# Kernel tuning notes

Measured on AMD Instinct MI355X. Metric: run time of the kernel, lower is better.

Reference implementation:

```python
import jax, jax.numpy as jnp
import numpy as np

LRELU_GAIN = 2.0 ** 0.5  # util.lrelu_gain (assumed sqrt(2))
EPS = 1e-8


def upsample2_bilinear_ac(x):
    # F.upsample_bilinear == bilinear with align_corners=True, scale 2
    B, C, H, W = x.shape
    def lerp_axis(t, n, axis):
        c = jnp.arange(2 * n, dtype=jnp.float32) * (n - 1) / (2 * n - 1)
        i0 = jnp.floor(c).astype(jnp.int32)
        i1 = jnp.minimum(i0 + 1, n - 1)
        f = c - i0.astype(jnp.float32)
        a = jnp.take(t, i0, axis=axis)
        b = jnp.take(t, i1, axis=axis)
        shape = [1] * t.ndim
        shape[axis] = 2 * n
        f = f.reshape(shape)
        return a * (1.0 - f) + b * f
    x = lerp_axis(x, H, 2)
    x = lerp_axis(x, W, 3)
    return x


def conv1x1(x, weight, bias, gain):
    # Conv2dNormalizedLR with kernel_size=1: he = gain/sqrt(in)
    cin = weight.shape[1]
    he = gain / float(cin) ** 0.5
    y = jnp.einsum('bihw,oi->bohw', x, weight[:, :, 0, 0] * he)
    return y + bias[None, :, None, None]


def mod_conv3x3(x, weight, style, gain):
    # weight: [Cin, Cout, 3, 3]; style: [B, Cin]
    cin, cout, k, _ = weight.shape
    he = gain / float(cin * k * k) ** 0.5
    wmod = style[:, :, None, None, None] * (weight * he)[None]  # [B,Cin,Cout,k,k]
    # demodulation: normalize over (in, kh, kw) per out channel
    d = jax.lax.rsqrt(jnp.sum(wmod * wmod, axis=(1, 3, 4), keepdims=True) + EPS)
    wmod = wmod * d
    # conv_transpose2d(stride=1, pad=1, k=3) == conv2d with transposed+flipped kernel, pad=1
    kern = jnp.flip(jnp.transpose(wmod, (0, 2, 1, 3, 4)), axis=(3, 4))  # [B,Cout,Cin,k,k]
    def one(xb, kb):
        return jax.lax.conv_general_dilated(
            xb[None], kb, (1, 1), ((1, 1), (1, 1)),
            dimension_numbers=('NCHW', 'OIHW', 'NCHW'))[0]
    y = jax.vmap(one)(x, kern)
    return y * gain


def noise_affine(noise, w_s, b_s, w_b, b_b):
    # Baff*: 1x1 conv from 1 channel, gain=1 -> he=1
    ys = noise * w_s[None, :, 0, None, 0, None][:, :, :, 0] if False else noise * w_s[:, 0, 0, 0][None, :, None, None] + b_s[None, :, None, None]
    yb = noise * w_b[:, 0, 0, 0][None, :, None, None] + b_b[None, :, None, None]
    return ys, yb


def block_forward(x, w, noise1, noise2, conv1_w, bias1, conv2_w, bias2,
                  Aaff1_w, Aaff1_b, Aaff2_w, Aaff2_b,
                  Baff1s_w, Baff1s_b, Baff1b_w, Baff1b_b,
                  Baff2s_w, Baff2s_b, Baff2b_w, Baff2b_b,
                  rgb_w, rgb_b):
    x = upsample2_bilinear_ac(x)
    style1 = conv1x1(w, Aaff1_w, Aaff1_b, 1.0)[:, :, 0, 0]  # [B, Cin]
    x = mod_conv3x3(x, conv1_w, style1, LRELU_GAIN)
    ys, yb = noise_affine(noise1, Baff1s_w, Baff1s_b, Baff1b_w, Baff1b_b)
    x = x * ys + yb + bias1
    x = jax.nn.leaky_relu(x, 0.2)
    style2 = conv1x1(w, Aaff2_w, Aaff2_b, 1.0)[:, :, 0, 0]
    x = mod_conv3x3(x, conv2_w, style2, LRELU_GAIN)
    ys, yb = noise_affine(noise2, Baff2s_w, Baff2s_b, Baff2b_w, Baff2b_b)
    x = x * ys + yb + bias2
    x = jax.nn.leaky_relu(x, 0.2)
    rgb = conv1x1(x, rgb_w, rgb_b, 0.03)
    return x, rgb


def setup_inputs() -> dict:
    key = jax.random.key(0)
    ks = jax.random.split(key, 20)
    B, Cin, Cout, Wd, H, W = 8, 512, 512, 512, 32, 32
    inp = {
        'x': jax.random.normal(ks[0], (B, Cin, H, W), jnp.float32),
        'w': jax.random.normal(ks[1], (B, Wd, 1, 1), jnp.float32),
        'noise1': jax.random.normal(ks[2], (B, 1, 2 * H, 2 * W), jnp.float32),
        'noise2': jax.random.normal(ks[3], (B, 1, 2 * H, 2 * W), jnp.float32),
        'conv1_w': jax.random.normal(ks[4], (Cin, Cout, 3, 3), jnp.float32),
        'bias1': jnp.zeros((1, Cout, 1, 1), jnp.float32),
        'conv2_w': jax.random.normal(ks[5], (Cout, Cout, 3, 3), jnp.float32),
        'bias2': jnp.zeros((1, Cout, 1, 1), jnp.float32),
        'Aaff1_w': jax.random.normal(ks[6], (Cin, Wd, 1, 1), jnp.float32),
        'Aaff1_b': jnp.zeros((Cin,), jnp.float32),
        'Aaff2_w': jax.random.normal(ks[7], (Cout, Wd, 1, 1), jnp.float32),
        'Aaff2_b': jnp.zeros((Cout,), jnp.float32),
        'Baff1s_w': jax.random.normal(ks[8], (Cout, 1, 1, 1), jnp.float32) * 0.1,
        'Baff1s_b': jnp.ones((Cout,), jnp.float32),
        'Baff1b_w': jax.random.normal(ks[9], (Cout, 1, 1, 1), jnp.float32) * 0.1,
        'Baff1b_b': jnp.zeros((Cout,), jnp.float32),
        'Baff2s_w': jax.random.normal(ks[10], (Cout, 1, 1, 1), jnp.float32) * 0.1,
        'Baff2s_b': jnp.ones((Cout,), jnp.float32),
        'Baff2b_w': jax.random.normal(ks[11], (Cout, 1, 1, 1), jnp.float32) * 0.1,
        'Baff2b_b': jnp.zeros((Cout,), jnp.float32),
        'rgb_w': jax.random.normal(ks[12], (3, Cout, 1, 1), jnp.float32),
        'rgb_b': jnp.zeros((3,), jnp.float32),
    }
    return inp


def reference(x, w, noise1, noise2, conv1_w, bias1, conv2_w, bias2,
              Aaff1_w, Aaff1_b, Aaff2_w, Aaff2_b,
              Baff1s_w, Baff1s_b, Baff1b_w, Baff1b_b,
              Baff2s_w, Baff2s_b, Baff2b_w, Baff2b_b,
              rgb_w, rgb_b):
    return block_forward(x, w, noise1, noise2, conv1_w, bias1, conv2_w, bias2,
                         Aaff1_w, Aaff1_b, Aaff2_w, Aaff2_b,
                         Baff1s_w, Baff1s_b, Baff1b_w, Baff1b_b,
                         Baff2s_w, Baff2s_b, Baff2b_w, Baff2b_b,
                         rgb_w, rgb_b)
```

## Files before the change

kernel.cpp:

```cpp
#include <hip/hip_runtime.h>
#include <hip/hip_bf16.h>

#define BB 8
#define CC 512
#define HO 64
#define HP 66
#define NPIX (BB*HO*HO)

typedef float f32x4 __attribute__((ext_vector_type(4)));
typedef __bf16 bf16x8 __attribute__((ext_vector_type(8)));
using bf16 = __hip_bfloat16;

__device__ __forceinline__ void gload16(const void* g, void* l) {
    __builtin_amdgcn_global_load_lds((const __attribute__((address_space(1))) void*)g,
                                     (__attribute__((address_space(3))) void*)l, 16, 0, 0);
}

__device__ __forceinline__ float waveRedSum(float v) {
    #pragma unroll
    for (int off = 32; off; off >>= 1) v += __shfl_down(v, off);
    return v;
}

__global__ void init_all(const float* __restrict__ W1, const float* __restrict__ W2,
                         float* __restrict__ S21, float* __restrict__ S22,
                         bf16* __restrict__ kT1, bf16* __restrict__ kT2, float he,
                         bf16* __restrict__ xs1, bf16* __restrict__ xs2,
                         const float* __restrict__ rgbb, float* __restrict__ outrgb) {
    int blk = blockIdx.x, tid = threadIdx.x;
    if (blk < 2048) {
        int which = blk >> 10;
        const float* Wsrc = which ? W2 : W1;
        float* S2ho = which ? S22 : S21;
        bf16* keffT = which ? kT2 : kT1;
        int t = ((blk & 1023) << 8) + tid;
        int i = t & (CC-1), o = t >> 9;
        const float* wp = Wsrc + (i*CC + o)*9;
        float v[9]; float s2 = 0.f;
        #pragma unroll
        for (int k = 0; k < 9; ++k) { v[k] = wp[k] * he; s2 += v[k]*v[k]; }
        S2ho[o*CC + i] = s2;
        #pragma unroll
        for (int tp = 0; tp < 9; ++tp) keffT[(tp*CC + o)*CC + i] = (bf16)v[8 - tp];
    } else if (blk < 3088) {
        int sub = ((blk - 2048) << 2) + (tid >> 6);
        int ln = tid & 63;
        bf16* dst = (sub & 1) ? xs2 : xs1;
        int idx = sub >> 1;
        int b = idx / 260, rm = idx - b*260;
        int p, q;
        if (rm < 66)       { p = 0;        q = rm; }
        else if (rm < 132) { p = 65;       q = rm - 66; }
        else if (rm < 196) { p = rm - 131; q = 0; }
        else               { p = rm - 195; q = 65; }
        f32x4* d4 = (f32x4*)(dst + ((size_t)((b*HP + p)*HP + q)) * CC);
        d4[ln] = f32x4{0.f, 0.f, 0.f, 0.f};
    } else {
        int t2 = ((blk - 3088) << 2) + (tid >> 6);
        int plane = t2 >> 4;
        int c = plane - (plane/3)*3;
        float v = rgbb[c];
        *(f32x4*)(outrgb + (plane << 12) + ((t2 & 15) << 8) + ((tid & 63) << 2)) =
            f32x4{v, v, v, v};
    }
}

__global__ void style_kernel(const float* __restrict__ w,
                             const float* __restrict__ A1, const float* __restrict__ A1b,
                             const float* __restrict__ A2, const float* __restrict__ A2b,
                             float* __restrict__ s1, float* __restrict__ s2) {
    int wid = (blockIdx.x * blockDim.x + threadIdx.x) >> 6;
    int lane = threadIdx.x & 63;
    int set = wid >= BB*CC; int rem = set ? wid - BB*CC : wid;
    int b = rem >> 9, i = rem & (CC-1);
    const float* A = set ? A2 : A1;
    const float* wb = w + b*CC;
    float sum = 0.f;
    for (int d = lane; d < CC; d += 64) sum += wb[d] * A[i*CC + d];
    sum = waveRedSum(sum);
    if (lane == 0) {
        float r = sum * 0.04419417382415922f + (set ? A2b : A1b)[i];
        (set ? s2 : s1)[b*CC + i] = r;
    }
}

__global__ void demod_kernel(const float* __restrict__ s1, const float* __restrict__ S21,
                             const float* __restrict__ s2, const float* __restrict__ S22,
                             float* __restrict__ dg1, float* __restrict__ dg2, float gain) {
    int wid = (blockIdx.x * blockDim.x + threadIdx.x) >> 6;
    int lane = threadIdx.x & 63;
    int set = wid >= BB*CC; int rem = set ? wid - BB*CC : wid;
    int b = rem >> 9, o = rem & (CC-1);
    const float* st = (set ? s2 : s1) + b*CC;
    const float* S2 = (set ? S22 : S21) + o*CC;
    float sum = 0.f;
    for (int i = lane; i < CC; i += 64) { float sv = st[i]; sum += sv*sv*S2[i]; }
    sum = waveRedSum(sum);
    if (lane == 0) (set ? dg2 : dg1)[b*CC + o] = gain * rsqrtf(sum + 1e-8f);
}

__global__ void upsample_mod(const float* __restrict__ x, const float* __restrict__ s1,
                             bf16* __restrict__ xs1) {
    __shared__ float usl[32][CC];
    int blk = blockIdx.x;
    int i = threadIdx.x;
    int b = blk >> 6, p = blk & 63;
    const float scale = 31.0f / 63.0f;
    float chf = p * scale; int h0 = (int)chf; float fh = chf - h0; int h1 = min(h0 + 1, 31);
    const float* xb = x + ((size_t)(b*CC + i) << 10);
    #pragma unroll
    for (int k = 0; k < 8; ++k) {
        f32x4 r0 = *(const f32x4*)(xb + (h0 << 5) + (k << 2));
        f32x4 r1 = *(const f32x4*)(xb + (h1 << 5) + (k << 2));
        #pragma unroll
        for (int e = 0; e < 4; ++e)
            usl[(k << 2) + e][i] = r0[e]*(1.f - fh) + r1[e]*fh;
    }
    float sv = s1[b*CC + i];
    bf16* op = xs1 + ((size_t)((b*HP + p + 1)*HP + 1))*CC + i;
    #pragma unroll
    for (int q = 0; q < 64; ++q) {
        float cwf = q * scale; int w0 = (int)cwf; float fw = cwf - w0;
        int w1 = min(w0 + 1, 31);
        float v = (usl[w0][i]*(1.f - fw) + usl[w1][i]*fw) * sv;
        op[q*CC] = (bf16)v;
    }
}

#define SB  __builtin_amdgcn_sched_barrier(0)
#define BAR __builtin_amdgcn_s_barrier()
#define VMC(n)  asm volatile("s_waitcnt vmcnt(" #n ")" ::: "memory")
#define LGKM(n) asm volatile("s_waitcnt lgkmcnt(" #n ")" ::: "memory")

#define STAGE_A(d, h, U) do { \
    gload16((U) + aThr + (h)*(HP*1024),                 ldsA + (d)*32768 + (h)*16384); \
    gload16((U) + aThr + (h)*(HP*1024) + 2*(HP*1024),   ldsA + (d)*32768 + (h)*16384 + 8192); \
} while (0)

#define STAGE_B(d, h, U) do { \
    gload16((U) + bThr + (h)*32768,                     ldsB + (d)*32768 + (h)*16384); \
    gload16((U) + bThr + (h)*32768 + 131072,            ldsB + (d)*32768 + (h)*16384 + 8192); \
} while (0)

#define LOAD_A(d, fh) do { \
    _Pragma("unroll") \
    for (int fmq = 0; fmq < 4; ++fmq) { \
        afr[fmq][0] = *(const bf16x8*)(aRd + (d)*32768 + (fh)*16384 + fmq*2048 + swz0); \
        afr[fmq][1] = *(const bf16x8*)(aRd + (d)*32768 + (fh)*16384 + fmq*2048 + swz1); \
    } } while (0)

#define LOAD_B(d, nh) do { \
    _Pragma("unroll") \
    for (int fnq = 0; fnq < 2; ++fnq) { \
        bfr[nh][fnq][0] = *(const bf16x8*)(bRd + (d)*32768 + (nh)*16384 + fnq*2048 + swz0); \
        bfr[nh][fnq][1] = *(const bf16x8*)(bRd + (d)*32768 + (nh)*16384 + fnq*2048 + swz1); \
    } } while (0)

#define QUAD(fh, nh) do { \
    __builtin_amdgcn_s_setprio(1); \
    _Pragma("unroll") \
    for (int kc = 0; kc < 2; ++kc) \
    { _Pragma("unroll") \
      for (int fmq = 0; fmq < 4; ++fmq) \
      { _Pragma("unroll") \
        for (int fnq = 0; fnq < 2; ++fnq) \
            acc[(fh)*4+fmq][(nh)*2+fnq] = __builtin_amdgcn_mfma_f32_16x16x32_bf16( \
                afr[fmq][kc], bfr[nh][fnq][kc], acc[(fh)*4+fmq][(nh)*2+fnq], 0, 0, 0); } } \
    __builtin_amdgcn_s_setprio(0); } while (0)

#define PHSTEP(cur, nxt, aN1, bN1, aN2, g1, g3) do { \
     \
    LOAD_A(cur, 0); \
    LOAD_B(cur, 0); \
    if (g1) STAGE_B(nxt, 0, bN1); \
    LGKM(8); SB; BAR; LGKM(0); SB; \
    QUAD(0, 0); \
    VMC(4); SB; BAR; SB; \
     \
    LOAD_B(cur, 1); \
    if (g1) STAGE_B(nxt, 1, bN1); \
    SB; BAR; LGKM(0); SB; \
    QUAD(0, 1); \
    SB; BAR; SB; \
     \
    LOAD_A(cur, 1); \
    if (g1) STAGE_A(nxt, 1, aN1); \
    SB; BAR; LGKM(0); SB; \
    QUAD(1, 1); \
    SB; BAR; SB; \
     \
    if (g3) STAGE_A(cur, 0, aN2); \
    SB; BAR; SB; \
    QUAD(1, 0); \
    if (g3) { VMC(6); } else { VMC(0); } \
    SB; BAR; SB; \
} while (0)

#define CONV_COMMON \
    __shared__ __attribute__((aligned(16))) bf16 As[32768]; \
    __shared__ __attribute__((aligned(16))) bf16 Bs[32768]; \
    const int tid = threadIdx.x; \
    const int wave = tid >> 6, lane = tid & 63; \
    const int tileId = ((blockIdx.x & 7) << 5) + (blockIdx.x >> 3); \
    const int mtile = tileId >> 1, ntile = tileId & 1; \
    const int m0 = mtile << 8, n0 = ntile << 8; \
    const int b  = m0 >> 12; \
    const int p0 = (m0 & 4095) >> 6; \
    const int wm = wave >> 2, wn = wave & 3; \
    const int l15 = lane & 15; \
    const int srcSwz = (((tid & 7) ^ ((tid >> 3) & 7)) << 4); \
    const int aThr = ((tid >> 3) << 10) + srcSwz; \
    const int bThr = (((tid >> 8) & 1) << 16) + (((tid >> 3) & 31) << 10) + srcSwz; \
    char* const ldsA = (char*)As + tid*16; \
    char* const ldsB = (char*)Bs + tid*16; \
    const char* const aRd = (const char*)As + (((wm << 6) + l15) << 7); \
    const char* const bRd = (const char*)Bs + (((wn << 5) + l15) << 7); \
    const int swz0 = (((lane >> 4)    ) ^ (lane & 7)) << 4; \
    const int swz1 = (((lane >> 4) | 4) ^ (lane & 7)) << 4; \
    f32x4 acc[8][4]; \
    _Pragma("unroll") \
    for (int i_ = 0; i_ < 8; ++i_) \
        _Pragma("unroll") \
        for (int j_ = 0; j_ < 4; ++j_) acc[i_][j_] = f32x4{0.f, 0.f, 0.f, 0.f}; \
    bf16x8 afr[4][2], bfr[2][2][2]; \
    auto abase = [&](int st) -> const char* { \
        int t = st >> 3; int dh = (t*11) >> 5; int dw = t - dh*3; \
        return (const char*)xs + ((size_t)((b*HP + p0 + dh)*HP + dw) << 10) + ((st & 7) << 7); \
    }; \
    auto bbase = [&](int st) -> const char* { \
        int t = st >> 3; \
        return (const char*)keffT + ((size_t)(t*CC + n0) << 10) + ((st & 7) << 7); \
    }; \
    { \
        const char* a0 = abase(0); const char* b0 = bbase(0); const char* a1 = abase(1); \
        STAGE_A(0, 0, a0); \
        STAGE_B(0, 0, b0); \
        STAGE_B(0, 1, b0); \
        STAGE_A(0, 1, a0); \
        STAGE_A(1, 0, a1); \
        VMC(6); SB; BAR; SB; \
    } \
    _Pragma("unroll 1") \
    for (int it = 0; it < 36; ++it) { \
        const bool more = (it < 35); \
        const char* aE = abase(2*it + 1); const char* bE = bbase(2*it + 1); \
        const char* aO = abase(2*it + 2); const char* bO = bbase(2*it + 2); \
        const char* aO2 = abase(2*it + 3); \
        PHSTEP(0, 1, aE, bE, aO,  true, more); \
        PHSTEP(1, 0, aO, bO, aO2, more, more); \
    }

__global__ __launch_bounds__(512, 2) void conv_gemm1(
    const bf16* __restrict__ xs, const bf16* __restrict__ keffT,
    const float* __restrict__ dg, const float* __restrict__ noise,
    const float* __restrict__ nsw, const float* __restrict__ nsb,
    const float* __restrict__ nbw, const float* __restrict__ nbb,
    const float* __restrict__ biasv, const float* __restrict__ stnext,
    bf16* __restrict__ outb) {
    CONV_COMMON
    const float* dgb = dg + b*CC;
    int nIdx[4]; float pdg[4], pnsw[4], pnsb[4], pnbw[4], pnbb[4], pbias[4], pst[4];
    #pragma unroll
    for (int fn = 0; fn < 4; ++fn) {
        int n = n0 + (wn << 6) + (fn << 4) + l15;
        nIdx[fn] = n;
        pdg[fn] = dgb[n]; pnsw[fn] = nsw[n]; pnsb[fn] = nsb[n];
        pnbw[fn] = nbw[n]; pnbb[fn] = nbb[n]; pbias[fn] = biasv[n];
        pst[fn] = stnext[b*CC + n];
    }
    #pragma unroll
    for (int fm = 0; fm < 8; ++fm) {
        const int mbase = m0 + (wm << 7) + (fm << 4) + ((lane >> 4) << 2);
        const f32x4 nsv = *(const f32x4*)(noise + mbase);
        #pragma unroll
        for (int r = 0; r < 4; ++r) {
            int mloc = mbase + r;
            float ns = nsv[r];
            int prow = (mloc & 4095) >> 6, qcol = mloc & 63;
            #pragma unroll
            for (int fn = 0; fn < 4; ++fn) {
                float v = acc[fm][fn][r] * pdg[fn];
                v = v * (ns*pnsw[fn] + pnsb[fn]) + (ns*pnbw[fn] + pnbb[fn]) + pbias[fn];
                v = fmaxf(v, 0.2f*v);
                outb[(((b*HP) + prow + 1)*HP + (qcol + 1))*CC + nIdx[fn]] =
                    (bf16)(v * pst[fn]);
            }
        }
    }
}

__global__ __launch_bounds__(512, 2) void conv_gemm2(
    const bf16* __restrict__ xs, const bf16* __restrict__ keffT,
    const float* __restrict__ dg, const float* __restrict__ noise,
    const float* __restrict__ nsw, const float* __restrict__ nsb,
    const float* __restrict__ nbw, const float* __restrict__ nbb,
    const float* __restrict__ biasv, float* __restrict__ outf,
    const float* __restrict__ rgbwv, float* __restrict__ outrgb) {
    CONV_COMMON
    const float* dgb = dg + b*CC;
    int nIdx[4]; float pdg[4], pnsw[4], pnsb[4], pnbw[4], pnbb[4], pbias[4];
    float w0[4], w1[4], w2[4];
    const float heR = 0.03f * 0.04419417382415922f;
    #pragma unroll
    for (int fn = 0; fn < 4; ++fn) {
        int n = n0 + (wn << 6) + (fn << 4) + l15;
        nIdx[fn] = n;
        pdg[fn] = dgb[n]; pnsw[fn] = nsw[n]; pnsb[fn] = nsb[n];
        pnbw[fn] = nbw[n]; pnbb[fn] = nbb[n]; pbias[fn] = biasv[n];
        w0[fn] = rgbwv[n] * heR;
        w1[fn] = rgbwv[CC + n] * heR;
        w2[fn] = rgbwv[2*CC + n] * heR;
    }
    #pragma unroll
    for (int fm = 0; fm < 8; ++fm) {
        const int mbase = m0 + (wm << 7) + (fm << 4) + ((lane >> 4) << 2);
        const f32x4 nsv = *(const f32x4*)(noise + mbase);
        f32x4 pc0 = {0.f,0.f,0.f,0.f}, pc1 = {0.f,0.f,0.f,0.f}, pc2 = {0.f,0.f,0.f,0.f};
        #pragma unroll
        for (int fn = 0; fn < 4; ++fn) {
            f32x4 vv;
            #pragma unroll
            for (int r = 0; r < 4; ++r) {
                float ns = nsv[r];
                float v = acc[fm][fn][r] * pdg[fn];
                v = v * (ns*pnsw[fn] + pnsb[fn]) + (ns*pnbw[fn] + pnbb[fn]) + pbias[fn];
                vv[r] = fmaxf(v, 0.2f*v);
            }
            pc0 += vv * w0[fn]; pc1 += vv * w1[fn]; pc2 += vv * w2[fn];
            *(f32x4*)(outf + ((size_t)(b*CC + nIdx[fn]) << 12) + (mbase & 4095)) = vv;
        }
        #pragma unroll
        for (int r = 0; r < 4; ++r) {
            float a0 = pc0[r], a1 = pc1[r], a2 = pc2[r];
            #pragma unroll
            for (int mk = 1; mk < 16; mk <<= 1) {
                a0 += __shfl_xor(a0, mk);
                a1 += __shfl_xor(a1, mk);
                a2 += __shfl_xor(a2, mk);
            }
            if (l15 < 3) {
                float av = (l15 == 0) ? a0 : (l15 == 1) ? a1 : a2;
                int px = (mbase + r) & 4095;
                atomicAdd(outrgb + (b*3 + l15)*4096 + px, av);
            }
        }
    }
}

extern "C" void kernel_launch(void* const* d_in, const int* in_sizes, int n_in,
                              void* d_out, int out_size, void* d_ws, size_t ws_size,
                              hipStream_t stream) {
    const float* x      = (const float*)d_in[0];
    const float* w      = (const float*)d_in[1];
    const float* noise1 = (const float*)d_in[2];
    const float* noise2 = (const float*)d_in[3];
    const float* conv1w = (const float*)d_in[4];
    const float* bias1  = (const float*)d_in[5];
    const float* conv2w = (const float*)d_in[6];
    const float* bias2  = (const float*)d_in[7];
    const float* A1w = (const float*)d_in[8];
    const float* A1b = (const float*)d_in[9];
    const float* A2w = (const float*)d_in[10];
    const float* A2b = (const float*)d_in[11];
    const float* B1sw = (const float*)d_in[12];
    const float* B1sb = (const float*)d_in[13];
    const float* B1bw = (const float*)d_in[14];
    const float* B1bb = (const float*)d_in[15];
    const float* B2sw = (const float*)d_in[16];
    const float* B2sb = (const float*)d_in[17];
    const float* B2bw = (const float*)d_in[18];
    const float* B2bb = (const float*)d_in[19];
    const float* rgbw = (const float*)d_in[20];
    const float* rgbb = (const float*)d_in[21];

    char* ws = (char*)d_ws;
    size_t off = 0;
    auto alloc = [&](size_t bytes) { char* p = ws + off; off += (bytes + 255) & ~(size_t)255; return p; };
    const size_t xsBytes = (size_t)BB*HP*HP*CC*2;
    bf16* xs1 = (bf16*)alloc(xsBytes);
    bf16* xs2 = (bf16*)alloc(xsBytes);
    bf16* kT1 = (bf16*)alloc((size_t)9*CC*CC*2);
    bf16* kT2 = (bf16*)alloc((size_t)9*CC*CC*2);
    float* S21 = (float*)alloc((size_t)CC*CC*4);
    float* S22 = (float*)alloc((size_t)CC*CC*4);
    float* s1  = (float*)alloc(BB*CC*4);
    float* s2  = (float*)alloc(BB*CC*4);
    float* dg1 = (float*)alloc(BB*CC*4);
    float* dg2 = (float*)alloc(BB*CC*4);

    float* outx   = (float*)d_out;
    float* outrgb = outx + (size_t)BB*CC*HO*HO;

    const float gain = 1.41421356237309515f;
    const float he = gain / sqrtf(512.f * 9.f);
    init_all<<<3184, 256, 0, stream>>>(conv1w, conv2w, S21, S22, kT1, kT2, he,
                                       xs1, xs2, rgbb, outrgb);
    style_kernel<<<2*BB*CC/4, 256, 0, stream>>>(w, A1w, A1b, A2w, A2b, s1, s2);
    demod_kernel<<<2*BB*CC/4, 256, 0, stream>>>(s1, S21, s2, S22, dg1, dg2, gain);
    upsample_mod<<<BB*HO, CC, 0, stream>>>(x, s1, xs1);
    conv_gemm1<<<(NPIX/256)*(CC/256), 512, 0, stream>>>(
        xs1, kT1, dg1, noise1, B1sw, B1sb, B1bw, B1bb, bias1, s2, xs2);
    conv_gemm2<<<(NPIX/256)*(CC/256), 512, 0, stream>>>(
        xs2, kT2, dg2, noise2, B2sw, B2sb, B2bw, B2bb, bias2, outx, rgbw, outrgb);
}
```

Baseline: 323.7 us.

## Replace fine-grained 8-phase barrier pipeline with simple double-buffered k-step loop

Replaces the interleaved per-quadrant schedule, which staggered global-to-LDS staging across four phases with barriers and partial waitcnts, with a plain double-buffer loop. Each k-step issues all next-stage loads up front, computes all four quadrants, then waits for all loads and synchronizes with one barrier. This cuts barrier count and scheduling complexity but drops the fine-grained overlap and the early prefetch of the next A tile, and it leaves the per-quadrant LDS-read waits to the compiler.

Result: no change. 318.1 us, median of 2 (-1.7%).

```diff
diff --git a/kernel.cpp b/kernel.cpp
--- a/kernel.cpp
+++ b/kernel.cpp
@@ -130,7 +130,6 @@
 #define SB  __builtin_amdgcn_sched_barrier(0)
 #define BAR __builtin_amdgcn_s_barrier()
 #define VMC(n)  asm volatile("s_waitcnt vmcnt(" #n ")" ::: "memory")
-#define LGKM(n) asm volatile("s_waitcnt lgkmcnt(" #n ")" ::: "memory")
 
 #define STAGE_A(d, h, U) do { \
     gload16((U) + aThr + (h)*(HP*1024),                 ldsA + (d)*32768 + (h)*16384); \
@@ -168,32 +167,19 @@
                 afr[fmq][kc], bfr[nh][fnq][kc], acc[(fh)*4+fmq][(nh)*2+fnq], 0, 0, 0); } } \
     __builtin_amdgcn_s_setprio(0); } while (0)
 
-#define PHSTEP(cur, nxt, aN1, bN1, aN2, g1, g3) do { \
-     \
-    LOAD_A(cur, 0); \
-    LOAD_B(cur, 0); \
-    if (g1) STAGE_B(nxt, 0, bN1); \
-    LGKM(8); SB; BAR; LGKM(0); SB; \
+#define KSTEP(cur, nxt, aN, bN, doStage) do { \
+    if (doStage) { \
+        STAGE_A(nxt, 0, aN); STAGE_A(nxt, 1, aN); \
+        STAGE_B(nxt, 0, bN); STAGE_B(nxt, 1, bN); \
+    } \
+    LOAD_A(cur, 0); LOAD_B(cur, 0); \
     QUAD(0, 0); \
-    VMC(4); SB; BAR; SB; \
-     \
     LOAD_B(cur, 1); \
-    if (g1) STAGE_B(nxt, 1, bN1); \
-    SB; BAR; LGKM(0); SB; \
     QUAD(0, 1); \
-    SB; BAR; SB; \
-     \
     LOAD_A(cur, 1); \
-    if (g1) STAGE_A(nxt, 1, aN1); \
-    SB; BAR; LGKM(0); SB; \
     QUAD(1, 1); \
-    SB; BAR; SB; \
-     \
-    if (g3) STAGE_A(cur, 0, aN2); \
-    SB; BAR; SB; \
     QUAD(1, 0); \
-    if (g3) { VMC(6); } else { VMC(0); } \
-    SB; BAR; SB; \
+    VMC(0); SB; BAR; SB; \
 } while (0)
 
 #define CONV_COMMON \
@@ -232,22 +218,18 @@
         return (const char*)keffT + ((size_t)(t*CC + n0) << 10) + ((st & 7) << 7); \
     }; \
     { \
-        const char* a0 = abase(0); const char* b0 = bbase(0); const char* a1 = abase(1); \
-        STAGE_A(0, 0, a0); \
-        STAGE_B(0, 0, b0); \
-        STAGE_B(0, 1, b0); \
-        STAGE_A(0, 1, a0); \
-        STAGE_A(1, 0, a1); \
-        VMC(6); SB; BAR; SB; \
+        const char* a0 = abase(0); const char* b0 = bbase(0); \
+        STAGE_A(0, 0, a0); STAGE_A(0, 1, a0); \
+        STAGE_B(0, 0, b0); STAGE_B(0, 1, b0); \
+        VMC(0); SB; BAR; SB; \
     } \
     _Pragma("unroll 1") \
     for (int it = 0; it < 36; ++it) { \
         const bool more = (it < 35); \
         const char* aE = abase(2*it + 1); const char* bE = bbase(2*it + 1); \
         const char* aO = abase(2*it + 2); const char* bO = bbase(2*it + 2); \
-        const char* aO2 = abase(2*it + 3); \
-        PHSTEP(0, 1, aE, bE, aO,  true, more); \
-        PHSTEP(1, 0, aO, bO, aO2, more, more); \
+        KSTEP(0, 1, aE, bE, true); \
+        KSTEP(1, 0, aO, bO, more); \
     }
 
 __global__ __launch_bounds__(512, 2) void conv_gemm1(
```
